# Performance work log

Measured on AMD Instinct MI355X. Metric: run time of the kernel, lower is better.

The kernel has to match this reference:

```python
import jax, jax.numpy as jnp
import numpy as np

D = 1024       # latent_size
LW = 16        # leaf_width
DEPTH = 8      # tree depth
NN = 2**DEPTH - 1   # internal decision nodes
NL = 2**DEPTH       # leaves
B, S = 2, 1024


def _fff(x, nw, nb, w1, b1, w2, b2, act):
    """Hard-routed Fast FeedForward (eval mode).
    x: (B,S,D); nw: (NN,D); nb: (NN,); w1: (NL,D,LW); b1: (NL,LW);
    w2: (NL,LW,D); b2: (NL,D).
    """
    node = jnp.zeros(x.shape[:2], dtype=jnp.int32)
    for _ in range(DEPTH):
        logit = jnp.einsum('bsd,bsd->bs', x, nw[node]) + nb[node]
        node = 2 * node + 1 + (logit > 0).astype(jnp.int32)
    leaf = node - NN  # (B,S) in [0, NL)
    h = act(jnp.einsum('bsd,bsdl->bsl', x, w1[leaf]) + b1[leaf])
    return jnp.einsum('bsl,bsld->bsd', h, w2[leaf]) + b2[leaf]


def _forward(x,
             q_nw, q_nb, q_w1, q_b1, q_w2, q_b2,
             k_nw, k_nb, k_w1, k_b1, k_w2, k_b2,
             v_nw, v_nb, v_w1, v_b1, v_w2, v_b2,
             f_nw, f_nb, f_w1, f_b1, f_w2, f_b2):
    # manual norm (torch std is unbiased; note original divides by sqrt(std+eps))
    mu = jnp.mean(x, -1, keepdims=True)
    sd = jnp.std(x, -1, ddof=1, keepdims=True)
    xn = (x - mu) / jnp.sqrt(sd + 1e-5)
    relu = jax.nn.relu
    q = _fff(xn, q_nw, q_nb, q_w1, q_b1, q_w2, q_b2, relu)
    k = _fff(xn, k_nw, k_nb, k_w1, k_b1, k_w2, k_b2, relu)
    v = _fff(xn, v_nw, v_nb, v_w1, v_b1, v_w2, v_b2, relu)
    att = jax.nn.softmax(jnp.einsum('bqd,bkd->bqk', q, k) / jnp.sqrt(jnp.float32(D)), axis=-1)
    y = xn + jnp.einsum('bqk,bkd->bqd', att, v)
    gelu = lambda t: jax.nn.gelu(t, approximate=False)
    return y + _fff(y, f_nw, f_nb, f_w1, f_b1, f_w2, f_b2, gelu)


def _make_fff_params(key, scale_in, scale_leaf):
    ks = jax.random.split(key, 4)
    nw = jax.random.normal(ks[0], (NN, D), jnp.float32) * scale_in
    nb = jnp.zeros((NN,), jnp.float32)
    w1 = jax.random.normal(ks[1], (NL, D, LW), jnp.float32) * scale_in
    b1 = jax.random.normal(ks[2], (NL, LW), jnp.float32) * 0.01
    w2 = jax.random.normal(ks[3], (NL, LW, D), jnp.float32) * scale_leaf
    b2 = jnp.zeros((NL, D), jnp.float32)
    return nw, nb, w1, b1, w2, b2


def setup_inputs() -> dict:
    key = jax.random.key(0)
    kx, kq, kk, kv, kf = jax.random.split(key, 5)
    s_in = 1.0 / np.sqrt(D)
    s_lf = 1.0 / np.sqrt(LW)
    inp = {"x": jax.random.normal(kx, (B, S, D), jnp.float32)}
    for name, kk_ in (("q", kq), ("k", kk), ("v", kv), ("f", kf)):
        nw, nb, w1, b1, w2, b2 = _make_fff_params(kk_, s_in, s_lf)
        inp.update({f"{name}_nw": nw, f"{name}_nb": nb, f"{name}_w1": w1,
                    f"{name}_b1": b1, f"{name}_w2": w2, f"{name}_b2": b2})
    return inp


def reference(x,
              q_nw, q_nb, q_w1, q_b1, q_w2, q_b2,
              k_nw, k_nb, k_w1, k_b1, k_w2, k_b2,
              v_nw, v_nb, v_w1, v_b1, v_w2, v_b2,
              f_nw, f_nb, f_w1, f_b1, f_w2, f_b2):
    return _forward(x,
                    q_nw, q_nb, q_w1, q_b1, q_w2, q_b2,
                    k_nw, k_nb, k_w1, k_b1, k_w2, k_b2,
                    v_nw, v_nb, v_w1, v_b1, v_w2, v_b2,
                    f_nw, f_nb, f_w1, f_b1, f_w2, f_b2)
```

## Files before the change

### kernel.cpp

```cpp
#include <hip/hip_runtime.h>
#include <hip/hip_bf16.h>
#include <math.h>

#define DD 1024
#define LWW 16
#define NNODES 255
#define NLEAF 256
#define BB 2
#define SS 1024
#define NTOK (BB*SS)
#define PLANE ((size_t)NTOK * DD)
#define MS ((size_t)1024 * 1024)
#define MAXCHUNK 512
#define CH 8

typedef short bf16x8 __attribute__((ext_vector_type(8)));
typedef float f32x4 __attribute__((ext_vector_type(4)));

#define GLOBAL_AS __attribute__((address_space(1)))
#define LDS_AS __attribute__((address_space(3)))

__device__ __forceinline__ void gld_lds16(const void* g, void* l) {
  __builtin_amdgcn_global_load_lds((const GLOBAL_AS unsigned int*)g,
                                   (LDS_AS unsigned int*)l, 16, 0, 0);
}

__device__ __forceinline__ unsigned short f2bf(float f) {
  union { float f; unsigned int u; } v; v.f = f;
  unsigned int u = v.u;
  unsigned int lsb = (u >> 16) & 1u;
  u += 0x7fffu + lsb;
  return (unsigned short)(u >> 16);
}
__device__ __forceinline__ float bf2f(unsigned short h) {
  union { unsigned int u; float f; } v; v.u = ((unsigned int)h) << 16;
  return v.f;
}
__device__ __forceinline__ void split3(float a, unsigned short& h0,
                                       unsigned short& h1, unsigned short& h2) {
  h0 = f2bf(a);
  float r = a - bf2f(h0);
  h1 = f2bf(r);
  float r2 = r - bf2f(h1);
  h2 = f2bf(r2);
}

__global__ __launch_bounds__(256) void norm_kernel(const float* __restrict__ x,
                                                   float* __restrict__ xn) {
  int tok = blockIdx.x, tid = threadIdx.x;
  const float4 v = ((const float4*)(x + (size_t)tok * DD))[tid];
  double s = (double)v.x + (double)v.y + (double)v.z + (double)v.w;
  double s2 = (double)v.x * v.x + (double)v.y * v.y + (double)v.z * v.z + (double)v.w * v.w;
  for (int o = 32; o; o >>= 1) { s += __shfl_down(s, o); s2 += __shfl_down(s2, o); }
  __shared__ double rs[4], rs2[4];
  __shared__ float stats[2];
  int wid = tid >> 6, lane = tid & 63;
  if (lane == 0) { rs[wid] = s; rs2[wid] = s2; }
  __syncthreads();
  if (tid == 0) {
    double ts = rs[0] + rs[1] + rs[2] + rs[3];
    double ts2 = rs2[0] + rs2[1] + rs2[2] + rs2[3];
    double mu = ts / DD;
    double var = (ts2 - DD * mu * mu) / (DD - 1);
    if (var < 0) var = 0;
    double sd = sqrt(var);
    stats[0] = (float)mu;
    stats[1] = (float)(1.0 / sqrt(sd + 1e-5));
  }
  __syncthreads();
  float mu = stats[0], inv = stats[1];
  float4 o;
  o.x = (v.x - mu) * inv; o.y = (v.y - mu) * inv;
  o.z = (v.z - mu) * inv; o.w = (v.w - mu) * inv;
  ((float4*)(xn + (size_t)tok * DD))[tid] = o;
}

__global__ __launch_bounds__(256) void route_kernel(
    const float* __restrict__ xin,
    const float* nw0, const float* nb0,
    const float* nw1, const float* nb1,
    const float* nw2, const float* nb2,
    int* __restrict__ leaf_arr, int* __restrict__ hist, int ntree) {
  int tid = threadIdx.x, lane = tid & 63, wid = tid >> 6;
  int gw = blockIdx.x * 4 + wid;
  int tok = gw / ntree, tr = gw - tok * ntree;
  if (tok >= NTOK) return;
  const float* nws[3] = {nw0, nw1, nw2};
  const float* nbs[3] = {nb0, nb1, nb2};
  const float* nw = nws[tr];
  const float* nb = nbs[tr];
  f32x4 xq[4];
  const f32x4* xb = (const f32x4*)(xin + (size_t)tok * DD);
#pragma unroll
  for (int j = 0; j < 4; ++j) xq[j] = xb[lane + 64 * j];
  int node = 0;
#pragma unroll 1
  for (int step = 0; step < 8; ++step) {
    const f32x4* wb = (const f32x4*)(nw + (size_t)node * DD);
    double p = 0.0;
#pragma unroll
    for (int j = 0; j < 4; ++j) {
      f32x4 w = wb[lane + 64 * j];
      p += (double)xq[j][0] * w[0] + (double)xq[j][1] * w[1] +
           (double)xq[j][2] * w[2] + (double)xq[j][3] * w[3];
    }
#pragma unroll
    for (int o = 1; o < 64; o <<= 1) p += __shfl_xor(p, o);
    double logit = p + (double)nb[node];
    node = 2 * node + 1 + (logit > 0.0 ? 1 : 0);
  }
  if (lane == 0) {
    int leaf = node - NNODES;
    leaf_arr[(size_t)tr * NTOK + tok] = leaf;
    atomicAdd(&hist[tr * NLEAF + leaf], 1);
  }
}

__global__ __launch_bounds__(256) void scan_kernel(const int* __restrict__ hist,
                                                   int* __restrict__ offs,
                                                   int* __restrict__ cursor,
                                                   int4* __restrict__ desc,
                                                   int ntree, int tree0) {
  __shared__ int buf[256];
  __shared__ int dcnt;
  int tid = threadIdx.x;
  for (int tr = 0; tr < ntree; ++tr) {
    int slot = tree0 + tr;
    int v = hist[slot * NLEAF + tid];
    buf[tid] = v;
    if (tid == 0) dcnt = 0;
    __syncthreads();
    int run = v;
    for (int off = 1; off < 256; off <<= 1) {
      int add = (tid >= off) ? buf[tid - off] : 0;
      __syncthreads();
      run += add;
      buf[tid] = run;
      __syncthreads();
    }
    if (tid == 0) offs[slot * (NLEAF + 1)] = 0;
    offs[slot * (NLEAF + 1) + tid + 1] = run;
    cursor[slot * NLEAF + tid] = run - v;
    if (v > 0) {
      int k = (v + CH - 1) / CH;
      int base = atomicAdd(&dcnt, k);
      int lo = run - v;
      for (int j = 0; j < k; ++j) {
        int s = lo + j * CH;
        int e = min(run, s + CH);
        desc[slot * MAXCHUNK + base + j] = make_int4(tid, s, e, 0);
      }
    }
    __syncthreads();
  }
}

__global__ __launch_bounds__(256) void scatter_kernel(const int* __restrict__ leaf_arr,
                                                      int* __restrict__ cursor,
                                                      int* __restrict__ list,
                                                      int tree0, int ntree) {
  int tok = blockIdx.x * 256 + threadIdx.x;
  for (int tr = 0; tr < ntree; ++tr) {
    int slot = tree0 + tr;
    int leaf = leaf_arr[(size_t)slot * NTOK + tok];
    int pos = atomicAdd(&cursor[slot * NLEAF + leaf], 1);
    list[(size_t)slot * NTOK + pos] = tok;
  }
}

struct LeafW {
  const float* w1[3]; const float* b1[3]; const float* w2[3]; const float* b2[3];
  unsigned short* outs[3];
  float* out_res;
};

__global__ __launch_bounds__(256) void leafmlp_kernel(
    const float* __restrict__ xin,
    const int* __restrict__ list, const int4* __restrict__ desc,
    LeafW W, int tree0, int act) {
  int ty = blockIdx.y;
  int slot = tree0 + ty;
  int4 dsc = desc[slot * MAXCHUNK + blockIdx.x];
  int leaf = dsc.x;
  if (leaf < 0) return;
  int lo = dsc.y, hi = dsc.z;
  const int* L = list + (size_t)slot * NTOK;
  const float* W1 = W.w1[ty] + (size_t)leaf * DD * LWW;
  const float* B1 = W.b1[ty] + (size_t)leaf * LWW;
  const float* W2 = W.w2[ty] + (size_t)leaf * LWW * DD;
  const float* B2 = W.b2[ty] + (size_t)leaf * DD;
  unsigned short* osp = W.outs[ty];
  int tid = threadIdx.x;
  int seg = tid >> 4, col = tid & 15;

  __shared__ float xs[CH][16][68];
  __shared__ float hpart2[4][CH][17];
  __shared__ float hs[CH][16];

  f32x4 w2r[16];
#pragma unroll
  for (int l = 0; l < 16; ++l) w2r[l] = *(const f32x4*)(W2 + l * 1024 + tid * 4);
  f32x4 b2v = *(const f32x4*)(B2 + tid * 4);

  int toks[CH];
#pragma unroll
  for (int t = 0; t < CH; ++t) {
    int idx = lo + t;
    toks[t] = (idx < hi) ? L[idx] : -1;
    if (toks[t] >= 0) {
      float4 v = ((const float4*)(xin + (size_t)toks[t] * DD))[tid];
      *(float4*)&xs[t][seg][col * 4] = v;
    } else {
      float4 z = {0.f, 0.f, 0.f, 0.f};
      *(float4*)&xs[t][seg][col * 4] = z;
    }
  }
  __syncthreads();

  float part[CH];
#pragma unroll
  for (int t = 0; t < CH; ++t) part[t] = 0.f;
  const float* wp = W1 + seg * 1024 + col;
#pragma unroll 4
  for (int i4 = 0; i4 < 64; i4 += 4) {
    float w0 = wp[(i4 + 0) * 16], w1v = wp[(i4 + 1) * 16];
    float w2v = wp[(i4 + 2) * 16], w3v = wp[(i4 + 3) * 16];
#pragma unroll
    for (int t = 0; t < CH; ++t) {
      float4 xv4 = *(const float4*)&xs[t][seg][i4];
      part[t] = fmaf(xv4.x, w0, fmaf(xv4.y, w1v, fmaf(xv4.z, w2v, fmaf(xv4.w, w3v, part[t]))));
    }
  }
#pragma unroll
  for (int t = 0; t < CH; ++t) {
    float p = part[t];
    p += __shfl_xor(p, 16);
    p += __shfl_xor(p, 32);
    if ((tid & 48) == 0) hpart2[tid >> 6][t][col] = p;
  }
  __syncthreads();

  if (tid < 16 * CH) {
    int t = tid >> 4, c = tid & 15;
    float h = B1[c] + hpart2[0][t][c] + hpart2[1][t][c] + hpart2[2][t][c] + hpart2[3][t][c];
    if (act == 0) h = fmaxf(h, 0.f);
    else h = 0.5f * h * (1.f + erff(h * 0.70710678118654752f));
    hs[t][c] = h;
  }
  __syncthreads();

  f32x4 acc[CH];
#pragma unroll
  for (int t = 0; t < CH; ++t) acc[t] = b2v;
#pragma unroll
  for (int l = 0; l < 16; ++l) {
    f32x4 wv = w2r[l];
#pragma unroll
    for (int t = 0; t < CH; ++t) acc[t] += wv * hs[t][l];
  }
#pragma unroll
  for (int t = 0; t < CH; ++t) {
    if (toks[t] < 0) break;
    size_t off = (size_t)toks[t] * DD + tid * 4;
    if (osp) {
      ushort4 o0, o1, o2;
      split3(acc[t][0], o0.x, o1.x, o2.x);
      split3(acc[t][1], o0.y, o1.y, o2.y);
      split3(acc[t][2], o0.z, o1.z, o2.z);
      split3(acc[t][3], o0.w, o1.w, o2.w);
      *(ushort4*)(osp + off) = o0;
      *(ushort4*)(osp + PLANE + off) = o1;
      *(ushort4*)(osp + 2 * PLANE + off) = o2;
    } else {
      float4 o;
      o.x = xs[t][seg][col * 4 + 0] + acc[t][0];
      o.y = xs[t][seg][col * 4 + 1] + acc[t][1];
      o.z = xs[t][seg][col * 4 + 2] + acc[t][2];
      o.w = xs[t][seg][col * 4 + 3] + acc[t][3];
      *(float4*)(W.out_res + off) = o;
    }
  }
}

__global__ __launch_bounds__(256) void transpose_v(const unsigned short* __restrict__ v,
                                                   unsigned short* __restrict__ vt) {
  __shared__ unsigned short t[32][34];
  int b = blockIdx.z & 1, p = blockIdx.z >> 1;
  int s0 = blockIdx.x * 32, d0 = blockIdx.y * 32;
  int tx = threadIdx.x, ty = threadIdx.y;
  const unsigned short* vb = v + p * PLANE + (size_t)b * SS * DD;
  unsigned short* vtb = vt + p * PLANE + (size_t)b * DD * SS;
#pragma unroll
  for (int k = 0; k < 4; ++k) {
    int r = ty + 8 * k;
    t[r][tx] = vb[(size_t)(s0 + r) * DD + d0 + tx];
  }
  __syncthreads();
#pragma unroll
  for (int k = 0; k < 4; ++k) {
    int r = ty + 8 * k;
    vtb[(size_t)(d0 + r) * SS + s0 + tx] = t[tx][r];
  }
}

#define BKK 64
__global__ __launch_bounds__(256) void gemm_nt3(
    const unsigned short* __restrict__ A,
    const unsigned short* __restrict__ Bt,
    float* __restrict__ C,
    const float* __restrict__ addsrc,
    float scale) {
  __shared__ short As[3][64 * BKK];
  __shared__ short Bs[3][64 * BKK];
  int b = blockIdx.z;
  int m0 = blockIdx.x * 64, n0 = blockIdx.y * 64;
  int tid = threadIdx.x, lane = tid & 63, wid = tid >> 6;
  int wm = wid >> 1, wn = wid & 1;
  f32x4 acc[2][2] = {};

  int sk0 = (((lane & 7) ^ (lane >> 3)) * 8);
  int srow0 = wid * 8 + (lane >> 3);
  int fr = lane & 15;
  int r7 = fr & 7;

  const unsigned short* Ap[3];
  const unsigned short* Bp[3];
#pragma unroll
  for (int p = 0; p < 3; ++p) {
    Ap[p] = A + p * PLANE + b * MS;
    Bp[p] = Bt + p * PLANE + b * MS;
  }

  for (int kt = 0; kt < 1024 / BKK; ++kt) {
    int kbase = kt * BKK;
#pragma unroll
    for (int p = 0; p < 3; ++p) {
#pragma unroll
      for (int r = 0; r < 2; ++r) {
        int row = r * 32 + srow0;
        gld_lds16(Ap[p] + (size_t)(m0 + row) * 1024 + kbase + sk0, &As[p][(r * 32 + wid * 8) * BKK]);
        gld_lds16(Bp[p] + (size_t)(n0 + row) * 1024 + kbase + sk0, &Bs[p][(r * 32 + wid * 8) * BKK]);
      }
    }
    __syncthreads();
#pragma unroll
    for (int kk = 0; kk < 2; ++kk) {
      int fkc = (((kk * 4 + (lane >> 4)) ^ r7) * 8);
      bf16x8 af[3][2], bfr[3][2];
#pragma unroll
      for (int p = 0; p < 3; ++p) {
        af[p][0]  = *(const bf16x8*)&As[p][(wm * 32 + fr) * BKK + fkc];
        af[p][1]  = *(const bf16x8*)&As[p][(wm * 32 + 16 + fr) * BKK + fkc];
        bfr[p][0] = *(const bf16x8*)&Bs[p][(wn * 32 + fr) * BKK + fkc];
        bfr[p][1] = *(const bf16x8*)&Bs[p][(wn * 32 + 16 + fr) * BKK + fkc];
      }
#pragma unroll
      for (int mi = 0; mi < 2; ++mi)
#pragma unroll
        for (int ni = 0; ni < 2; ++ni) {
          acc[mi][ni] = __builtin_amdgcn_mfma_f32_16x16x32_bf16(af[2][mi], bfr[0][ni], acc[mi][ni], 0, 0, 0);
          acc[mi][ni] = __builtin_amdgcn_mfma_f32_16x16x32_bf16(af[1][mi], bfr[1][ni], acc[mi][ni], 0, 0, 0);
          acc[mi][ni] = __builtin_amdgcn_mfma_f32_16x16x32_bf16(af[0][mi], bfr[2][ni], acc[mi][ni], 0, 0, 0);
          acc[mi][ni] = __builtin_amdgcn_mfma_f32_16x16x32_bf16(af[1][mi], bfr[0][ni], acc[mi][ni], 0, 0, 0);
          acc[mi][ni] = __builtin_amdgcn_mfma_f32_16x16x32_bf16(af[0][mi], bfr[1][ni], acc[mi][ni], 0, 0, 0);
          acc[mi][ni] = __builtin_amdgcn_mfma_f32_16x16x32_bf16(af[0][mi], bfr[0][ni], acc[mi][ni], 0, 0, 0);
        }
    }
    __syncthreads();
  }

  float* Cb = C + b * MS;
  const float* Rb = addsrc ? addsrc + b * MS : nullptr;
  int crow0 = (lane >> 4) * 4, ccol = lane & 15;
#pragma unroll
  for (int mi = 0; mi < 2; ++mi)
#pragma unroll
    for (int ni = 0; ni < 2; ++ni) {
      int colg = n0 + wn * 32 + ni * 16 + ccol;
#pragma unroll
      for (int j = 0; j < 4; ++j) {
        int rowg = m0 + wm * 32 + mi * 16 + crow0 + j;
        float vv = acc[mi][ni][j] * scale;
        if (Rb) vv += Rb[(size_t)rowg * 1024 + colg];
        Cb[(size_t)rowg * 1024 + colg] = vv;
      }
    }
}

__global__ __launch_bounds__(256) void softmax_kernel(const float* __restrict__ sc,
                                                      unsigned short* __restrict__ P) {
  int row = blockIdx.x, tid = threadIdx.x;
  int wid = tid >> 6, lane = tid & 63;
  const float4 v = ((const float4*)(sc + (size_t)row * SS))[tid];
  float mx = fmaxf(fmaxf(v.x, v.y), fmaxf(v.z, v.w));
  for (int o = 32; o; o >>= 1) mx = fmaxf(mx, __shfl_down(mx, o));
  __shared__ float red[4];
  __shared__ float bres[2];
  if (lane == 0) red[wid] = mx;
  __syncthreads();
  if (tid == 0) bres[0] = fmaxf(fmaxf(red[0], red[1]), fmaxf(red[2], red[3]));
  __syncthreads();
  float m = bres[0];
  float e0 = expf(v.x - m), e1 = expf(v.y - m), e2 = expf(v.z - m), e3 = expf(v.w - m);
  float s = e0 + e1 + e2 + e3;
  for (int o = 32; o; o >>= 1) s += __shfl_down(s, o);
  if (lane == 0) red[wid] = s;
  __syncthreads();
  if (tid == 0) bres[1] = red[0] + red[1] + red[2] + red[3];
  __syncthreads();
  float inv = 1.f / bres[1];
  float p0 = e0 * inv, p1 = e1 * inv, p2 = e2 * inv, p3 = e3 * inv;
  ushort4 o0, o1, o2;
  split3(p0, o0.x, o1.x, o2.x);
  split3(p1, o0.y, o1.y, o2.y);
  split3(p2, o0.z, o1.z, o2.z);
  split3(p3, o0.w, o1.w, o2.w);
  size_t off = (size_t)row * SS + tid * 4;
  *(ushort4*)(P + off) = o0;
  *(ushort4*)(P + PLANE + off) = o1;
  *(ushort4*)(P + 2 * PLANE + off) = o2;
}

extern "C" void kernel_launch(void* const* d_in, const int* in_sizes, int n_in,
                              void* d_out, int out_size, void* d_ws, size_t ws_size,
                              hipStream_t stream) {
  const float* x = (const float*)d_in[0];
  const float* qp[6]; const float* kp[6]; const float* vp[6]; const float* fp[6];
  for (int i = 0; i < 6; ++i) {
    qp[i] = (const float*)d_in[1 + i];
    kp[i] = (const float*)d_in[7 + i];
    vp[i] = (const float*)d_in[13 + i];
    fp[i] = (const float*)d_in[19 + i];
  }
  char* ws = (char*)d_ws;
  float* xn           = (float*)(ws);
  unsigned short* qb  = (unsigned short*)(ws + ( 8 << 20));
  unsigned short* kb  = (unsigned short*)(ws + (20 << 20));
  unsigned short* vs  = (unsigned short*)(ws + (32 << 20));
  unsigned short* vt  = (unsigned short*)(ws + (44 << 20));
  float* sc           = (float*)(ws + (32 << 20));
  unsigned short* P   = (unsigned short*)(ws + ( 8 << 20));
  float* y            = (float*)(ws + (20 << 20));
  int* meta           = (int*)(ws + (56 << 20));
  int* hist           = meta;
  int* cursor         = meta + 1024;
  int* offs           = meta + 2048;
  int* leaf_arr       = meta + 4096;
  int* list           = meta + 12288;
  int4* desc          = (int4*)(meta + 20480);
  float* out          = (float*)d_out;

  hipMemsetAsync(hist, 0, 1024 * sizeof(int), stream);
  hipMemsetAsync(desc, 0xFF, 4 * MAXCHUNK * sizeof(int4), stream);
  norm_kernel<<<NTOK, 256, 0, stream>>>(x, xn);
  route_kernel<<<NTOK * 3 / 4, 256, 0, stream>>>(xn, qp[0], qp[1], kp[0], kp[1], vp[0], vp[1],
                                                 leaf_arr, hist, 3);
  scan_kernel<<<1, 256, 0, stream>>>(hist, offs, cursor, desc, 3, 0);
  scatter_kernel<<<NTOK / 256, 256, 0, stream>>>(leaf_arr, cursor, list, 0, 3);

  LeafW Wqkv;
  Wqkv.w1[0] = qp[2]; Wqkv.b1[0] = qp[3]; Wqkv.w2[0] = qp[4]; Wqkv.b2[0] = qp[5];
  Wqkv.w1[1] = kp[2]; Wqkv.b1[1] = kp[3]; Wqkv.w2[1] = kp[4]; Wqkv.b2[1] = kp[5];
  Wqkv.w1[2] = vp[2]; Wqkv.b1[2] = vp[3]; Wqkv.w2[2] = vp[4]; Wqkv.b2[2] = vp[5];
  Wqkv.outs[0] = qb; Wqkv.outs[1] = kb; Wqkv.outs[2] = vs;
  Wqkv.out_res = nullptr;
  leafmlp_kernel<<<dim3(MAXCHUNK, 3), 256, 0, stream>>>(xn, list, desc, Wqkv, 0, 0);

  transpose_v<<<dim3(32, 32, 6), dim3(32, 8), 0, stream>>>(vs, vt);
  gemm_nt3<<<dim3(16, 16, 2), 256, 0, stream>>>(qb, kb, sc, nullptr, 0.03125f);
  softmax_kernel<<<NTOK, 256, 0, stream>>>(sc, P);
  gemm_nt3<<<dim3(16, 16, 2), 256, 0, stream>>>(P, vt, y, xn, 1.0f);

  route_kernel<<<NTOK / 4, 256, 0, stream>>>(y, fp[0], fp[1], fp[0], fp[1], fp[0], fp[1],
                                             leaf_arr + 3 * NTOK, hist + 3 * NLEAF, 1);
  scan_kernel<<<1, 256, 0, stream>>>(hist, offs, cursor, desc, 1, 3);
  scatter_kernel<<<NTOK / 256, 256, 0, stream>>>(leaf_arr, cursor, list, 3, 1);

  LeafW Wf;
  Wf.w1[0] = fp[2]; Wf.b1[0] = fp[3]; Wf.w2[0] = fp[4]; Wf.b2[0] = fp[5];
  Wf.w1[1] = fp[2]; Wf.b1[1] = fp[3]; Wf.w2[1] = fp[4]; Wf.b2[1] = fp[5];
  Wf.w1[2] = fp[2]; Wf.b1[2] = fp[3]; Wf.w2[2] = fp[4]; Wf.b2[2] = fp[5];
  Wf.outs[0] = nullptr; Wf.outs[1] = nullptr; Wf.outs[2] = nullptr;
  Wf.out_res = out;
  leafmlp_kernel<<<dim3(MAXCHUNK, 1), 256, 0, stream>>>(y, list, desc, Wf, 3, 1);
}
```

Baseline: 205.4 us.

## Stream leaf MLP weights through double-buffered LDS with async global-to-LDS loads

```diff
diff --git a/kernel.cpp b/kernel.cpp
--- a/kernel.cpp
+++ b/kernel.cpp
@@ -191,77 +191,124 @@
   const float* B2 = W.b2[ty] + (size_t)leaf * DD;
   unsigned short* osp = W.outs[ty];
   int tid = threadIdx.x;
-  int seg = tid >> 4, col = tid & 15;
-
-  __shared__ float xs[CH][16][68];
+  int lane = tid & 63, wid = tid >> 6;
+  int g = tid >> 4, c = tid & 15;
+
+  __shared__ float xsl[CH][1024];
+  __shared__ float wbuf[2][2048];
   __shared__ float hpart2[4][CH][17];
   __shared__ float hs[CH][16];
 
-  f32x4 w2r[16];
-#pragma unroll
-  for (int l = 0; l < 16; ++l) w2r[l] = *(const f32x4*)(W2 + l * 1024 + tid * 4);
-  f32x4 b2v = *(const f32x4*)(B2 + tid * 4);
-
-  int toks[CH];
+  int toks[CH], wtok[CH];
 #pragma unroll
   for (int t = 0; t < CH; ++t) {
     int idx = lo + t;
-    toks[t] = (idx < hi) ? L[idx] : -1;
-    if (toks[t] >= 0) {
-      float4 v = ((const float4*)(xin + (size_t)toks[t] * DD))[tid];
-      *(float4*)&xs[t][seg][col * 4] = v;
-    } else {
-      float4 z = {0.f, 0.f, 0.f, 0.f};
-      *(float4*)&xs[t][seg][col * 4] = z;
-    }
-  }
+    int v = (idx < hi) ? L[idx] : -1;
+    wtok[t] = v;
+    toks[t] = (v >= 0) ? v : L[lo];
+  }
+  float b1c = B1[c];
+  f32x4 b2v = *(const f32x4*)(B2 + tid * 4);
+  asm volatile("s_waitcnt vmcnt(0)" ::: "memory");
+
+#pragma unroll
+  for (int t = 0; t < CH; ++t)
+    gld_lds16(xin + (size_t)toks[t] * DD + wid * 256 + lane * 4, &xsl[t][wid * 256]);
+#pragma unroll
+  for (int s = 0; s < 2; ++s)
+#pragma unroll
+    for (int j = 0; j < 2; ++j)
+      gld_lds16(W1 + s * 2048 + wid * 512 + j * 256 + lane * 4,
+                &wbuf[s][wid * 512 + j * 256]);
+  asm volatile("s_waitcnt vmcnt(2)" ::: "memory");
   __syncthreads();
 
   float part[CH];
 #pragma unroll
   for (int t = 0; t < CH; ++t) part[t] = 0.f;
-  const float* wp = W1 + seg * 1024 + col;
-#pragma unroll 4
-  for (int i4 = 0; i4 < 64; i4 += 4) {
-    float w0 = wp[(i4 + 0) * 16], w1v = wp[(i4 + 1) * 16];
-    float w2v = wp[(i4 + 2) * 16], w3v = wp[(i4 + 3) * 16];
-#pragma unroll
-    for (int t = 0; t < CH; ++t) {
-      float4 xv4 = *(const float4*)&xs[t][seg][i4];
-      part[t] = fmaf(xv4.x, w0, fmaf(xv4.y, w1v, fmaf(xv4.z, w2v, fmaf(xv4.w, w3v, part[t]))));
-    }
-  }
+#pragma unroll
+  for (int sl = 0; sl < 8; ++sl) {
+    int cur = sl & 1;
+#pragma unroll
+    for (int q = 0; q < 2; ++q) {
+      int r0 = g * 8 + q * 4;
+      float w0 = wbuf[cur][(r0 + 0) * 16 + c];
+      float w1v = wbuf[cur][(r0 + 1) * 16 + c];
+      float w2v = wbuf[cur][(r0 + 2) * 16 + c];
+      float w3v = wbuf[cur][(r0 + 3) * 16 + c];
+      int xi = sl * 128 + r0;
+#pragma unroll
+      for (int t = 0; t < CH; ++t) {
+        f32x4 xq = *(const f32x4*)&xsl[t][xi];
+        part[t] = fmaf(xq[0], w0, fmaf(xq[1], w1v, fmaf(xq[2], w2v, fmaf(xq[3], w3v, part[t]))));
+      }
+    }
+    asm volatile("s_waitcnt lgkmcnt(0)" ::: "memory");
+    if (sl < 6) {
+#pragma unroll
+      for (int j = 0; j < 2; ++j)
+        gld_lds16(W1 + (sl + 2) * 2048 + wid * 512 + j * 256 + lane * 4,
+                  &wbuf[cur][wid * 512 + j * 256]);
+      asm volatile("s_waitcnt vmcnt(2)" ::: "memory");
+    } else if (sl < 7) {
+      asm volatile("s_waitcnt vmcnt(0)" ::: "memory");
+    }
+  }
+
 #pragma unroll
   for (int t = 0; t < CH; ++t) {
     float p = part[t];
     p += __shfl_xor(p, 16);
     p += __shfl_xor(p, 32);
-    if ((tid & 48) == 0) hpart2[tid >> 6][t][col] = p;
-  }
-  __syncthreads();
-
+    if ((tid & 48) == 0) hpart2[wid][t][c] = p;
+  }
+  __syncthreads();
   if (tid < 16 * CH) {
-    int t = tid >> 4, c = tid & 15;
-    float h = B1[c] + hpart2[0][t][c] + hpart2[1][t][c] + hpart2[2][t][c] + hpart2[3][t][c];
+    int t = tid >> 4;
+    float h = b1c + hpart2[0][t][c] + hpart2[1][t][c] + hpart2[2][t][c] + hpart2[3][t][c];
     if (act == 0) h = fmaxf(h, 0.f);
     else h = 0.5f * h * (1.f + erff(h * 0.70710678118654752f));
     hs[t][c] = h;
   }
   __syncthreads();
 
+#pragma unroll
+  for (int s = 0; s < 2; ++s)
+#pragma unroll
+    for (int l = 0; l < 2; ++l)
+      gld_lds16(W2 + (size_t)(s * 2 + l) * 1024 + wid * 256 + lane * 4,
+                &wbuf[s][l * 1024 + wid * 256]);
+  asm volatile("s_waitcnt vmcnt(2)" ::: "memory");
+
   f32x4 acc[CH];
 #pragma unroll
   for (int t = 0; t < CH; ++t) acc[t] = b2v;
 #pragma unroll
-  for (int l = 0; l < 16; ++l) {
-    f32x4 wv = w2r[l];
-#pragma unroll
-    for (int t = 0; t < CH; ++t) acc[t] += wv * hs[t][l];
-  }
+  for (int sl = 0; sl < 8; ++sl) {
+    int cur = sl & 1;
+#pragma unroll
+    for (int l = 0; l < 2; ++l) {
+      f32x4 wv = *(const f32x4*)&wbuf[cur][l * 1024 + tid * 4];
+      int lg = sl * 2 + l;
+#pragma unroll
+      for (int t = 0; t < CH; ++t) acc[t] += wv * hs[t][lg];
+    }
+    asm volatile("s_waitcnt lgkmcnt(0)" ::: "memory");
+    if (sl < 6) {
+#pragma unroll
+      for (int l = 0; l < 2; ++l)
+        gld_lds16(W2 + (size_t)((sl + 2) * 2 + l) * 1024 + wid * 256 + lane * 4,
+                  &wbuf[cur][l * 1024 + wid * 256]);
+      asm volatile("s_waitcnt vmcnt(2)" ::: "memory");
+    } else if (sl < 7) {
+      asm volatile("s_waitcnt vmcnt(0)" ::: "memory");
+    }
+  }
+
 #pragma unroll
   for (int t = 0; t < CH; ++t) {
-    if (toks[t] < 0) break;
-    size_t off = (size_t)toks[t] * DD + tid * 4;
+    if (wtok[t] < 0) break;
+    size_t off = (size_t)wtok[t] * DD + tid * 4;
     if (osp) {
       ushort4 o0, o1, o2;
       split3(acc[t][0], o0.x, o1.x, o2.x);
@@ -272,11 +319,12 @@
       *(ushort4*)(osp + PLANE + off) = o1;
       *(ushort4*)(osp + 2 * PLANE + off) = o2;
     } else {
+      float4 xr = *(const float4*)&xsl[t][tid * 4];
       float4 o;
-      o.x = xs[t][seg][col * 4 + 0] + acc[t][0];
-      o.y = xs[t][seg][col * 4 + 1] + acc[t][1];
-      o.z = xs[t][seg][col * 4 + 2] + acc[t][2];
-      o.w = xs[t][seg][col * 4 + 3] + acc[t][3];
+      o.x = xr.x + acc[t][0];
+      o.y = xr.y + acc[t][1];
+      o.z = xr.z + acc[t][2];
+      o.w = xr.w + acc[t][3];
       *(float4*)(W.out_res + off) = o;
     }
   }
```

Result: slower. 234.1 us (+14.0%).

## Restructure leaf MLP W1 loads as coalesced float4 with prefetch and split W2 loads

Applied to the files above, without the earlier changes.

```diff
diff --git a/kernel.cpp b/kernel.cpp
--- a/kernel.cpp
+++ b/kernel.cpp
@@ -191,16 +191,13 @@
   const float* B2 = W.b2[ty] + (size_t)leaf * DD;
   unsigned short* osp = W.outs[ty];
   int tid = threadIdx.x;
-  int seg = tid >> 4, col = tid & 15;
-
-  __shared__ float xs[CH][16][68];
-  __shared__ float hpart2[4][CH][17];
+  int lane = tid & 63, wid = tid >> 6;
+
+  __shared__ float xsl[CH][1024];
+  __shared__ float hpart[4][CH][20];
   __shared__ float hs[CH][16];
 
-  f32x4 w2r[16];
-#pragma unroll
-  for (int l = 0; l < 16; ++l) w2r[l] = *(const f32x4*)(W2 + l * 1024 + tid * 4);
-  f32x4 b2v = *(const f32x4*)(B2 + tid * 4);
+  float b1c = B1[tid & 15];
 
   int toks[CH];
 #pragma unroll
@@ -209,55 +206,89 @@
     toks[t] = (idx < hi) ? L[idx] : -1;
     if (toks[t] >= 0) {
       float4 v = ((const float4*)(xin + (size_t)toks[t] * DD))[tid];
-      *(float4*)&xs[t][seg][col * 4] = v;
+      *(float4*)&xsl[t][tid * 4] = v;
     } else {
       float4 z = {0.f, 0.f, 0.f, 0.f};
-      *(float4*)&xs[t][seg][col * 4] = z;
-    }
-  }
-  __syncthreads();
-
-  float part[CH];
-#pragma unroll
-  for (int t = 0; t < CH; ++t) part[t] = 0.f;
-  const float* wp = W1 + seg * 1024 + col;
-#pragma unroll 4
-  for (int i4 = 0; i4 < 64; i4 += 4) {
-    float w0 = wp[(i4 + 0) * 16], w1v = wp[(i4 + 1) * 16];
-    float w2v = wp[(i4 + 2) * 16], w3v = wp[(i4 + 3) * 16];
-#pragma unroll
-    for (int t = 0; t < CH; ++t) {
-      float4 xv4 = *(const float4*)&xs[t][seg][i4];
-      part[t] = fmaf(xv4.x, w0, fmaf(xv4.y, w1v, fmaf(xv4.z, w2v, fmaf(xv4.w, w3v, part[t]))));
-    }
-  }
+      *(float4*)&xsl[t][tid * 4] = z;
+    }
+  }
+  __syncthreads();
+
+  int r = tid >> 2;
+  const float* W1p = W1 + (size_t)r * 16 + (tid & 3) * 4;
+  f32x4 part4[CH];
+#pragma unroll
+  for (int t = 0; t < CH; ++t) part4[t] = (f32x4){0.f, 0.f, 0.f, 0.f};
+
+  f32x4 wv[4], wn[4];
+#pragma unroll
+  for (int j = 0; j < 4; ++j) wv[j] = *(const f32x4*)(W1p + (size_t)j * 1024);
+#pragma unroll
+  for (int pg = 0; pg < 4; ++pg) {
+    if (pg < 3) {
+#pragma unroll
+      for (int j = 0; j < 4; ++j)
+        wn[j] = *(const f32x4*)(W1p + (size_t)((pg + 1) * 4 + j) * 1024);
+    }
+#pragma unroll
+    for (int j = 0; j < 4; ++j) {
+      int p = pg * 4 + j;
+#pragma unroll
+      for (int t = 0; t < CH; ++t) {
+        float xv = xsl[t][p * 64 + r];
+        part4[t] += xv * wv[j];
+      }
+    }
+#pragma unroll
+    for (int j = 0; j < 4; ++j) wv[j] = wn[j];
+  }
+
+  const float* W2p = W2 + tid * 4;
+  f32x4 w2a[8];
+#pragma unroll
+  for (int l = 0; l < 8; ++l) w2a[l] = *(const f32x4*)(W2p + (size_t)l * 1024);
+  f32x4 b2v = *(const f32x4*)(B2 + tid * 4);
+
 #pragma unroll
   for (int t = 0; t < CH; ++t) {
-    float p = part[t];
-    p += __shfl_xor(p, 16);
-    p += __shfl_xor(p, 32);
-    if ((tid & 48) == 0) hpart2[tid >> 6][t][col] = p;
+    f32x4 v = part4[t];
+#pragma unroll
+    for (int o = 4; o < 64; o <<= 1) {
+      v[0] += __shfl_xor(v[0], o);
+      v[1] += __shfl_xor(v[1], o);
+      v[2] += __shfl_xor(v[2], o);
+      v[3] += __shfl_xor(v[3], o);
+    }
+    if (lane < 4) *(f32x4*)&hpart[wid][t][lane * 4] = v;
   }
   __syncthreads();
 
   if (tid < 16 * CH) {
     int t = tid >> 4, c = tid & 15;
-    float h = B1[c] + hpart2[0][t][c] + hpart2[1][t][c] + hpart2[2][t][c] + hpart2[3][t][c];
+    float h = b1c + hpart[0][t][c] + hpart[1][t][c] + hpart[2][t][c] + hpart[3][t][c];
     if (act == 0) h = fmaxf(h, 0.f);
     else h = 0.5f * h * (1.f + erff(h * 0.70710678118654752f));
     hs[t][c] = h;
   }
   __syncthreads();
 
+  f32x4 w2b[8];
+#pragma unroll
+  for (int l = 0; l < 8; ++l) w2b[l] = *(const f32x4*)(W2p + (size_t)(8 + l) * 1024);
   f32x4 acc[CH];
 #pragma unroll
   for (int t = 0; t < CH; ++t) acc[t] = b2v;
 #pragma unroll
-  for (int l = 0; l < 16; ++l) {
-    f32x4 wv = w2r[l];
-#pragma unroll
-    for (int t = 0; t < CH; ++t) acc[t] += wv * hs[t][l];
-  }
+  for (int l = 0; l < 8; ++l) {
+#pragma unroll
+    for (int t = 0; t < CH; ++t) acc[t] += w2a[l] * hs[t][l];
+  }
+#pragma unroll
+  for (int l = 0; l < 8; ++l) {
+#pragma unroll
+    for (int t = 0; t < CH; ++t) acc[t] += w2b[l] * hs[t][8 + l];
+  }
+
 #pragma unroll
   for (int t = 0; t < CH; ++t) {
     if (toks[t] < 0) break;
@@ -272,11 +303,12 @@
       *(ushort4*)(osp + PLANE + off) = o1;
       *(ushort4*)(osp + 2 * PLANE + off) = o2;
     } else {
+      float4 xr = *(const float4*)&xsl[t][tid * 4];
       float4 o;
-      o.x = xs[t][seg][col * 4 + 0] + acc[t][0];
-      o.y = xs[t][seg][col * 4 + 1] + acc[t][1];
-      o.z = xs[t][seg][col * 4 + 2] + acc[t][2];
-      o.w = xs[t][seg][col * 4 + 3] + acc[t][3];
+      o.x = xr.x + acc[t][0];
+      o.y = xr.y + acc[t][1];
+      o.z = xr.z + acc[t][2];
+      o.w = xr.w + acc[t][3];
       *(float4*)(W.out_res + off) = o;
     }
   }
```

New measurement: 186.9 us. 1.1x faster.
